# Optimization experiments

Hardware: AMD Instinct MI355X
Metric: run time of the kernel (lower is better)

Reference implementation:

```python
import jax, jax.numpy as jnp
import numpy as np

BATCH = 2048
TEMP = 0.5
EPS = 1e-12  # matches F.normalize default eps


def setup_inputs() -> dict:
    key = jax.random.key(0)
    k1, k2 = jax.random.split(key)
    emb_i = jax.random.normal(k1, (BATCH, 256), dtype=jnp.float32)
    emb_j = jax.random.normal(k2, (BATCH, 256), dtype=jnp.float32)
    return {"emb_i": emb_i, "emb_j": emb_j}


def _l2_normalize(x):
    norm = jnp.sqrt(jnp.sum(x * x, axis=1, keepdims=True))
    return x / jnp.maximum(norm, EPS)


def reference(emb_i, emb_j):
    n = emb_i.shape[0]  # = BATCH
    z_i = _l2_normalize(emb_i)
    z_j = _l2_normalize(emb_j)
    z = jnp.concatenate([z_i, z_j], axis=0)            # [2N, D]
    # cosine similarity of normalized vectors == plain GEMM
    sim = jnp.einsum('id,jd->ij', z, z)                # [2N, 2N]
    # positive pairs: diag offsets +N and -N
    sim_i_j = jnp.diagonal(sim, offset=n)              # [N]
    sim_j_i = jnp.diagonal(sim, offset=-n)             # [N]
    positives = jnp.concatenate([sim_i_j, sim_j_i])    # [2N]
    neg_mask = 1.0 - jnp.eye(2 * n, dtype=sim.dtype)   # [2N, 2N]
    numerator = jnp.exp(positives / TEMP)
    denominator = jnp.sum(neg_mask * jnp.exp(sim / TEMP), axis=1)  # [2N]
    loss_partial = -jnp.log(numerator / denominator)
    return jnp.sum(loss_partial) / (2 * n)
```

## Files before the change

kernel.cpp:

```cpp
#include <hip/hip_runtime.h>
#include <hip/hip_bf16.h>
#include <math.h>

#define NB        2048
#define TWO_N     4096
#define DIM       256
#define EPS       1e-12f
#define NT1D      (TWO_N / 128)
#define NTILES    (NT1D * (NT1D + 1) / 2)


typedef __attribute__((ext_vector_type(8))) short  bf16x8;
typedef __attribute__((ext_vector_type(4))) float  f32x4;

__global__ __launch_bounds__(256) void nrm_kernel(
    const float* __restrict__ emb_i, const float* __restrict__ emb_j,
    short* __restrict__ zt, float* __restrict__ pos,
    float* __restrict__ out)
{
    int t = threadIdx.x;
    int wave = t >> 6, lane = t & 63;
    int r = blockIdx.x * 4 + wave;
    float4 a = ((const float4*)(emb_i + (size_t)r * DIM))[lane];
    float4 b = ((const float4*)(emb_j + (size_t)r * DIM))[lane];
    float sa = a.x*a.x + a.y*a.y + a.z*a.z + a.w*a.w;
    float sb = b.x*b.x + b.y*b.y + b.z*b.z + b.w*b.w;
    float sd = a.x*b.x + a.y*b.y + a.z*b.z + a.w*b.w;
    #pragma unroll
    for (int off = 32; off >= 1; off >>= 1) {
        sa += __shfl_xor(sa, off, 64);
        sb += __shfl_xor(sb, off, 64);
        sd += __shfl_xor(sd, off, 64);
    }
    float si = 1.0f / fmaxf(sqrtf(sa), EPS);
    float sj = 1.0f / fmaxf(sqrtf(sb), EPS);

    int dst = (r >> 4) * 4096 + (lane >> 3) * 512 + ((lane >> 1) & 3) * 128
            + (r & 15) * 8 + (lane & 1) * 4;

    union { __hip_bfloat16 h[4]; uint2 u; } pk;
    pk.h[0] = __float2bfloat16(a.x * si);
    pk.h[1] = __float2bfloat16(a.y * si);
    pk.h[2] = __float2bfloat16(a.z * si);
    pk.h[3] = __float2bfloat16(a.w * si);
    *(uint2*)(zt + dst) = pk.u;
    pk.h[0] = __float2bfloat16(b.x * sj);
    pk.h[1] = __float2bfloat16(b.y * sj);
    pk.h[2] = __float2bfloat16(b.z * sj);
    pk.h[3] = __float2bfloat16(b.w * sj);
    *(uint2*)(zt + dst + 128 * 4096) = pk.u;

    if (lane == 0) pos[r] = sd * si * sj;
    if (blockIdx.x == 0 && t == 0) out[0] = 0.0f;
}

#define MFMA1(Av, Bv, m, n) \
    acc[m][n] = __builtin_amdgcn_mfma_f32_16x16x32_bf16(Av, Bv, acc[m][n], 0, 0, 0);

#define MFMA_ROW(Av, B0v, B1v, B2v, B3v, m) \
    MFMA1(Av, B0v, m, 0) MFMA1(Av, B1v, m, 1) \
    MFMA1(Av, B2v, m, 2) MFMA1(Av, B3v, m, 3)

#define MMSTEP(A0v, A1v, A2v, A3v, B0v, B1v, B2v, B3v) \
    MFMA_ROW(A0v, B0v, B1v, B2v, B3v, 0) \
    MFMA_ROW(A1v, B0v, B1v, B2v, B3v, 1) \
    MFMA_ROW(A2v, B0v, B1v, B2v, B3v, 2) \
    MFMA_ROW(A3v, B0v, B1v, B2v, B3v, 3)

#define LDSET(dA0, dA1, dA2, dA3, dB0, dB1, dB2, dB3, s) \
    dA0 = *(const bf16x8*)(apt0 + (s) * 512); \
    dA1 = *(const bf16x8*)(apt1 + (s) * 512); \
    dA2 = *(const bf16x8*)(apt2 + (s) * 512); \
    dA3 = *(const bf16x8*)(apt3 + (s) * 512); \
    dB0 = *(const bf16x8*)(bpt0 + (s) * 512); \
    dB1 = *(const bf16x8*)(bpt1 + (s) * 512); \
    dB2 = *(const bf16x8*)(bpt2 + (s) * 512); \
    dB3 = *(const bf16x8*)(bpt3 + (s) * 512);

#define SB __builtin_amdgcn_sched_barrier(0);

__global__ __launch_bounds__(256, 2) void simexp_kernel(
    const short* __restrict__ zt, float* __restrict__ part)
{
    int id = blockIdx.x;
    int by = (int)((sqrtf(8.0f * (float)id + 1.0f) - 1.0f) * 0.5f);
    while ((by + 1) * (by + 2) / 2 <= id) ++by;
    while (by * (by + 1) / 2 > id) --by;
    int bx = id - by * (by + 1) / 2;

    const short* Z = zt;
    int t = threadIdx.x;
    int w = t >> 6, lane = t & 63;
    int quad = lane >> 4, c16 = lane & 15;
    int wm = w >> 1, wn = w & 1;
    int rbase = bx * 128 + wm * 64;
    int jbase = by * 128 + wn * 64;

    const short* apt0 = Z + (size_t)((rbase >> 4) + 0) * 4096 + lane * 8;
    const short* apt1 = Z + (size_t)((rbase >> 4) + 1) * 4096 + lane * 8;
    const short* apt2 = Z + (size_t)((rbase >> 4) + 2) * 4096 + lane * 8;
    const short* apt3 = Z + (size_t)((rbase >> 4) + 3) * 4096 + lane * 8;
    const short* bpt0 = Z + (size_t)((jbase >> 4) + 0) * 4096 + lane * 8;
    const short* bpt1 = Z + (size_t)((jbase >> 4) + 1) * 4096 + lane * 8;
    const short* bpt2 = Z + (size_t)((jbase >> 4) + 2) * 4096 + lane * 8;
    const short* bpt3 = Z + (size_t)((jbase >> 4) + 3) * 4096 + lane * 8;

    f32x4 acc[4][4];
    #pragma unroll
    for (int mt = 0; mt < 4; ++mt)
        #pragma unroll
        for (int nt = 0; nt < 4; ++nt)
            acc[mt][nt] = (f32x4){0.f, 0.f, 0.f, 0.f};

    bf16x8 A0, A1, A2, A3, B0, B1, B2, B3;
    bf16x8 P0, P1, P2, P3, Q0, Q1, Q2, Q3;
    bf16x8 R0, R1, R2, R3, S0, S1, S2, S3;
    bf16x8 U0, U1, U2, U3, V0, V1, V2, V3;

    LDSET(A0, A1, A2, A3, B0, B1, B2, B3, 0)
    LDSET(P0, P1, P2, P3, Q0, Q1, Q2, Q3, 1)
    LDSET(R0, R1, R2, R3, S0, S1, S2, S3, 2)
    LDSET(U0, U1, U2, U3, V0, V1, V2, V3, 3)
    SB
    MMSTEP(A0, A1, A2, A3, B0, B1, B2, B3)
    SB
    LDSET(A0, A1, A2, A3, B0, B1, B2, B3, 4)
    SB
    MMSTEP(P0, P1, P2, P3, Q0, Q1, Q2, Q3)
    SB
    LDSET(P0, P1, P2, P3, Q0, Q1, Q2, Q3, 5)
    SB
    MMSTEP(R0, R1, R2, R3, S0, S1, S2, S3)
    SB
    LDSET(R0, R1, R2, R3, S0, S1, S2, S3, 6)
    SB
    MMSTEP(U0, U1, U2, U3, V0, V1, V2, V3)
    SB
    LDSET(U0, U1, U2, U3, V0, V1, V2, V3, 7)
    SB
    MMSTEP(A0, A1, A2, A3, B0, B1, B2, B3)
    MMSTEP(P0, P1, P2, P3, Q0, Q1, Q2, Q3)
    MMSTEP(R0, R1, R2, R3, S0, S1, S2, S3)
    MMSTEP(U0, U1, U2, U3, V0, V1, V2, V3)

    float rsum[4][4];
    #pragma unroll
    for (int mt = 0; mt < 4; ++mt)
        #pragma unroll
        for (int rg = 0; rg < 4; ++rg) rsum[mt][rg] = 0.f;

    if (bx == by) {
        #pragma unroll
        for (int mt = 0; mt < 4; ++mt) {
            #pragma unroll
            for (int nt = 0; nt < 4; ++nt) {
                int j = jbase + nt * 16 + c16;
                #pragma unroll
                for (int rg = 0; rg < 4; ++rg) {
                    int r = rbase + mt * 16 + quad * 4 + rg;
                    float e = __expf(2.0f * acc[mt][nt][rg]);
                    rsum[mt][rg] += (r == j) ? 0.f : e;
                }
            }
        }
    } else {
        float csum[4] = {0.f, 0.f, 0.f, 0.f};
        #pragma unroll
        for (int mt = 0; mt < 4; ++mt) {
            #pragma unroll
            for (int nt = 0; nt < 4; ++nt) {
                #pragma unroll
                for (int rg = 0; rg < 4; ++rg) {
                    float e = __expf(2.0f * acc[mt][nt][rg]);
                    rsum[mt][rg] += e;
                    csum[nt] += e;
                }
            }
        }
        #pragma unroll
        for (int nt = 0; nt < 4; ++nt) {
            float v = csum[nt];
            v += __shfl_xor(v, 16, 64);
            v += __shfl_xor(v, 32, 64);
            if (quad == 0)
                part[(size_t)(by * 128 + wn * 64 + nt * 16 + c16) * 64
                     + 2 * bx + wm] = v;
        }
    }

    #pragma unroll
    for (int mt = 0; mt < 4; ++mt) {
        #pragma unroll
        for (int rg = 0; rg < 4; ++rg) {
            float v = rsum[mt][rg];
            v += __shfl_xor(v, 1, 64);
            v += __shfl_xor(v, 2, 64);
            v += __shfl_xor(v, 4, 64);
            v += __shfl_xor(v, 8, 64);
            if (c16 == 0)
                part[(size_t)(rbase + mt * 16 + quad * 4 + rg) * 64
                     + 2 * by + wn] = v;
        }
    }
}

__global__ __launch_bounds__(128) void redloss_kernel(
    const float* __restrict__ part, const float* __restrict__ pos,
    float* __restrict__ out)
{
    int s = blockIdx.x, t = threadIdx.x;
    int r = s * 128 + t;
    const float4* p = (const float4*)(part + ((size_t)r << 6));
    float sum = 0.f;
    #pragma unroll
    for (int i = 0; i < 16; ++i) {
        float4 v = p[i];
        sum += v.x + v.y + v.z + v.w;
    }
    float val = logf(sum) - 2.0f * pos[r & (NB - 1)];
    #pragma unroll
    for (int off = 32; off >= 1; off >>= 1) val += __shfl_xor(val, off, 64);
    __shared__ float red[2];
    if ((t & 63) == 0) red[t >> 6] = val;
    __syncthreads();
    if (t == 0)
        atomicAdd(out, (red[0] + red[1]) * (1.0f / (float)TWO_N));
}

extern "C" void kernel_launch(void* const* d_in, const int* in_sizes, int n_in,
                              void* d_out, int out_size, void* d_ws, size_t ws_size,
                              hipStream_t stream)
{
    const float* emb_i = (const float*)d_in[0];
    const float* emb_j = (const float*)d_in[1];
    float* out = (float*)d_out;

    short* zt = (short*)d_ws;
    float* part = (float*)((char*)d_ws + (size_t)TWO_N * DIM * sizeof(short));
    float* pos = part + (size_t)TWO_N * 64;

    nrm_kernel<<<NB / 4, 256, 0, stream>>>(emb_i, emb_j, zt, pos, out);
    simexp_kernel<<<NTILES, 256, 0, stream>>>(zt, part);
    redloss_kernel<<<NT1D, 128, 0, stream>>>(part, pos, out);
}
```

Measured before the change: 77.39 us.

## Stage GEMM operand tiles through double-buffered LDS shared across waves

```diff
diff --git a/kernel.cpp b/kernel.cpp
--- a/kernel.cpp
+++ b/kernel.cpp
@@ -67,43 +67,66 @@
     MFMA_ROW(A2v, B0v, B1v, B2v, B3v, 2) \
     MFMA_ROW(A3v, B0v, B1v, B2v, B3v, 3)
 
-#define LDSET(dA0, dA1, dA2, dA3, dB0, dB1, dB2, dB3, s) \
-    dA0 = *(const bf16x8*)(apt0 + (s) * 512); \
-    dA1 = *(const bf16x8*)(apt1 + (s) * 512); \
-    dA2 = *(const bf16x8*)(apt2 + (s) * 512); \
-    dA3 = *(const bf16x8*)(apt3 + (s) * 512); \
-    dB0 = *(const bf16x8*)(bpt0 + (s) * 512); \
-    dB1 = *(const bf16x8*)(bpt1 + (s) * 512); \
-    dB2 = *(const bf16x8*)(bpt2 + (s) * 512); \
-    dB3 = *(const bf16x8*)(bpt3 + (s) * 512);
-
 #define SB __builtin_amdgcn_sched_barrier(0);
+
+#define SLD(c) \
+    G0 = *(const bf16x8*)(stg_base + 0 * 4096 + (2*(c)+0) * 512); \
+    G1 = *(const bf16x8*)(stg_base + 0 * 4096 + (2*(c)+1) * 512); \
+    G2 = *(const bf16x8*)(stg_base + 1 * 4096 + (2*(c)+0) * 512); \
+    G3 = *(const bf16x8*)(stg_base + 1 * 4096 + (2*(c)+1) * 512); \
+    G4 = *(const bf16x8*)(stg_base + 2 * 4096 + (2*(c)+0) * 512); \
+    G5 = *(const bf16x8*)(stg_base + 2 * 4096 + (2*(c)+1) * 512); \
+    G6 = *(const bf16x8*)(stg_base + 3 * 4096 + (2*(c)+0) * 512); \
+    G7 = *(const bf16x8*)(stg_base + 3 * 4096 + (2*(c)+1) * 512);
+
+#define DSW(bs) \
+    *(bf16x8*)&lds[(bs)*16384 + (p0+0)*512 + l8] = G0; \
+    *(bf16x8*)&lds[(bs)*16384 + (p0+1)*512 + l8] = G1; \
+    *(bf16x8*)&lds[(bs)*16384 + (p0+2)*512 + l8] = G2; \
+    *(bf16x8*)&lds[(bs)*16384 + (p0+3)*512 + l8] = G3; \
+    *(bf16x8*)&lds[(bs)*16384 + (p0+4)*512 + l8] = G4; \
+    *(bf16x8*)&lds[(bs)*16384 + (p0+5)*512 + l8] = G5; \
+    *(bf16x8*)&lds[(bs)*16384 + (p0+6)*512 + l8] = G6; \
+    *(bf16x8*)&lds[(bs)*16384 + (p0+7)*512 + l8] = G7;
+
+#define CSTEP(bs, sl) \
+    { \
+        bf16x8 fa0 = *(const bf16x8*)&lds[(bs)*16384 + ((wm4+0)*2+(sl))*512 + l8]; \
+        bf16x8 fa1 = *(const bf16x8*)&lds[(bs)*16384 + ((wm4+1)*2+(sl))*512 + l8]; \
+        bf16x8 fa2 = *(const bf16x8*)&lds[(bs)*16384 + ((wm4+2)*2+(sl))*512 + l8]; \
+        bf16x8 fa3 = *(const bf16x8*)&lds[(bs)*16384 + ((wm4+3)*2+(sl))*512 + l8]; \
+        bf16x8 fb0 = *(const bf16x8*)&lds[(bs)*16384 + 8192 + ((wn4+0)*2+(sl))*512 + l8]; \
+        bf16x8 fb1 = *(const bf16x8*)&lds[(bs)*16384 + 8192 + ((wn4+1)*2+(sl))*512 + l8]; \
+        bf16x8 fb2 = *(const bf16x8*)&lds[(bs)*16384 + 8192 + ((wn4+2)*2+(sl))*512 + l8]; \
+        bf16x8 fb3 = *(const bf16x8*)&lds[(bs)*16384 + 8192 + ((wn4+3)*2+(sl))*512 + l8]; \
+        MMSTEP(fa0, fa1, fa2, fa3, fb0, fb1, fb2, fb3) \
+    }
+
+#define COMPUTE(bs) CSTEP(bs, 0) CSTEP(bs, 1)
 
 __global__ __launch_bounds__(256, 2) void simexp_kernel(
     const short* __restrict__ zt, float* __restrict__ part)
 {
+    __shared__ short lds[2 * 16384];
+
     int id = blockIdx.x;
     int by = (int)((sqrtf(8.0f * (float)id + 1.0f) - 1.0f) * 0.5f);
     while ((by + 1) * (by + 2) / 2 <= id) ++by;
     while (by * (by + 1) / 2 > id) --by;
     int bx = id - by * (by + 1) / 2;
 
-    const short* Z = zt;
     int t = threadIdx.x;
     int w = t >> 6, lane = t & 63;
     int quad = lane >> 4, c16 = lane & 15;
     int wm = w >> 1, wn = w & 1;
+    int wm4 = wm * 4, wn4 = wn * 4;
+    int l8 = lane * 8;
+    int p0 = w * 8;
     int rbase = bx * 128 + wm * 64;
     int jbase = by * 128 + wn * 64;
 
-    const short* apt0 = Z + (size_t)((rbase >> 4) + 0) * 4096 + lane * 8;
-    const short* apt1 = Z + (size_t)((rbase >> 4) + 1) * 4096 + lane * 8;
-    const short* apt2 = Z + (size_t)((rbase >> 4) + 2) * 4096 + lane * 8;
-    const short* apt3 = Z + (size_t)((rbase >> 4) + 3) * 4096 + lane * 8;
-    const short* bpt0 = Z + (size_t)((jbase >> 4) + 0) * 4096 + lane * 8;
-    const short* bpt1 = Z + (size_t)((jbase >> 4) + 1) * 4096 + lane * 8;
-    const short* bpt2 = Z + (size_t)((jbase >> 4) + 2) * 4096 + lane * 8;
-    const short* bpt3 = Z + (size_t)((jbase >> 4) + 3) * 4096 + lane * 8;
+    const short* stg_base = zt
+        + (size_t)((w < 2 ? bx : by) * 8 + (w & 1) * 4) * 4096 + l8;
 
     f32x4 acc[4][4];
     #pragma unroll
@@ -112,36 +135,24 @@
         for (int nt = 0; nt < 4; ++nt)
             acc[mt][nt] = (f32x4){0.f, 0.f, 0.f, 0.f};
 
-    bf16x8 A0, A1, A2, A3, B0, B1, B2, B3;
-    bf16x8 P0, P1, P2, P3, Q0, Q1, Q2, Q3;
-    bf16x8 R0, R1, R2, R3, S0, S1, S2, S3;
-    bf16x8 U0, U1, U2, U3, V0, V1, V2, V3;
-
-    LDSET(A0, A1, A2, A3, B0, B1, B2, B3, 0)
-    LDSET(P0, P1, P2, P3, Q0, Q1, Q2, Q3, 1)
-    LDSET(R0, R1, R2, R3, S0, S1, S2, S3, 2)
-    LDSET(U0, U1, U2, U3, V0, V1, V2, V3, 3)
-    SB
-    MMSTEP(A0, A1, A2, A3, B0, B1, B2, B3)
-    SB
-    LDSET(A0, A1, A2, A3, B0, B1, B2, B3, 4)
-    SB
-    MMSTEP(P0, P1, P2, P3, Q0, Q1, Q2, Q3)
-    SB
-    LDSET(P0, P1, P2, P3, Q0, Q1, Q2, Q3, 5)
-    SB
-    MMSTEP(R0, R1, R2, R3, S0, S1, S2, S3)
-    SB
-    LDSET(R0, R1, R2, R3, S0, S1, S2, S3, 6)
-    SB
-    MMSTEP(U0, U1, U2, U3, V0, V1, V2, V3)
-    SB
-    LDSET(U0, U1, U2, U3, V0, V1, V2, V3, 7)
-    SB
-    MMSTEP(A0, A1, A2, A3, B0, B1, B2, B3)
-    MMSTEP(P0, P1, P2, P3, Q0, Q1, Q2, Q3)
-    MMSTEP(R0, R1, R2, R3, S0, S1, S2, S3)
-    MMSTEP(U0, U1, U2, U3, V0, V1, V2, V3)
+    bf16x8 G0, G1, G2, G3, G4, G5, G6, G7;
+
+    SLD(0)
+    DSW(0)
+    __syncthreads();
+    SLD(1) SB
+    COMPUTE(0) SB
+    DSW(1)
+    __syncthreads();
+    SLD(2) SB
+    COMPUTE(1) SB
+    DSW(0)
+    __syncthreads();
+    SLD(3) SB
+    COMPUTE(0)   SB
+    DSW(1)
+    __syncthreads();
+    COMPUTE(1)
 
     float rsum[4][4];
     #pragma unroll
```

Result: no change. 76.89 us (-0.6%).
